# Performance work log

Hardware: AMD Instinct MI355X
Metric: run time of the kernel (lower is better)

## Reference

```python
import jax, jax.numpy as jnp
import numpy as np

NUM_NODES = 100000
OUT_CHANNELS = 32
NUM_EDGES = 3200000


def setup_inputs() -> dict:
    key = jax.random.key(0)
    k1, k2, k3 = jax.random.split(key, 3)
    edge_index = jax.random.randint(k1, (2, NUM_EDGES), 0, NUM_NODES, dtype=jnp.int64)
    # nn.Linear init: weight [out, in], uniform(-1/sqrt(in), 1/sqrt(in))
    bound = 1.0 / np.sqrt(NUM_NODES)
    W = jax.random.uniform(k2, (OUT_CHANNELS, NUM_NODES), jnp.float32, -bound, bound)
    b = jax.random.uniform(k3, (OUT_CHANNELS,), jnp.float32, -bound, bound)
    return {"edge_index": edge_index, "W": W, "b": b}


def reference(edge_index, W, b):
    # LINK forward: A = sparse COO [N, num_nodes] with 1.0 per edge (duplicates sum),
    # logits = A @ W.T + b. Implemented as gather + segment_sum (no dense A).
    row = edge_index[0]
    col = edge_index[1]
    row = row - row.min()  # faithful to `row = row - row.min()`
    gathered = jnp.take(W.T, col, axis=0)  # [E, out_channels]
    logits = jax.ops.segment_sum(gathered, row, num_segments=NUM_NODES)  # [N, out]
    return logits + b
```

## Files before the change

### kernel.cpp

```cpp
#include <hip/hip_runtime.h>

#define NUM_NODES 100000
#define OUT_CH 32
#define NUM_EDGES 3200000

#define RPB 128
#define NB 782
#define CAP2 5120
#define TPB 512
#define TILE 12800
#define KPT 25
#define NTILE 250
#define TR_BLOCKS 3125
#define MIN_BLOCKS 256

static __device__ __forceinline__ unsigned short f32_to_bf16_rne(float f) {
    unsigned u = __float_as_uint(f);
    unsigned r = u + 0x7FFFu + ((u >> 16) & 1u);
    return (unsigned short)(r >> 16);
}
static __device__ __forceinline__ float bf16_to_f32(unsigned short h) {
    return __uint_as_float(((unsigned)h) << 16);
}

__global__ void __launch_bounds__(256)
fused_pre(const float* __restrict__ W, ushort4* __restrict__ Wt,
          const int4* __restrict__ row4, int* __restrict__ partmin,
          int* __restrict__ bcount) {
    int bk = blockIdx.x;
    int t  = threadIdx.x;
    if (bk < TR_BLOCKS) {
        __shared__ float tile[32][33];
        int tx = t & 31, ty = t >> 5;
        int colBase = bk * 32;
        #pragma unroll
        for (int k = 0; k < 4; k++) {
            int c = ty + 8 * k;
            tile[c][tx] = W[c * NUM_NODES + colBase + tx];
        }
        __syncthreads();
        int lc = t >> 3, q = t & 7;
        ushort4 o;
        o.x = f32_to_bf16_rne(tile[q * 4 + 0][lc]);
        o.y = f32_to_bf16_rne(tile[q * 4 + 1][lc]);
        o.z = f32_to_bf16_rne(tile[q * 4 + 2][lc]);
        o.w = f32_to_bf16_rne(tile[q * 4 + 3][lc]);
        Wt[(size_t)(colBase + lc) * 8 + q] = o;
    } else if (bk < TR_BLOCKS + MIN_BLOCKS) {
        int mb  = bk - TR_BLOCKS;
        int tid = mb * 256 + t;
        int m = 0x7fffffff;
        for (int i = tid; i < NUM_EDGES / 4; i += MIN_BLOCKS * 256) {
            int4 v = row4[i];
            m = min(m, min(min(v.x, v.y), min(v.z, v.w)));
        }
        #pragma unroll
        for (int off = 32; off > 0; off >>= 1) m = min(m, __shfl_down(m, off, 64));
        __shared__ int wm[4];
        if ((t & 63) == 0) wm[t >> 6] = m;
        __syncthreads();
        if (t == 0) partmin[mb] = min(min(wm[0], wm[1]), min(wm[2], wm[3]));
    } else {
        for (int i = t; i < NB; i += 256) bcount[i] = 0;
    }
}

__global__ void __launch_bounds__(TPB)
bin_stage(const int* __restrict__ edge, const int* __restrict__ partmin,
          int* __restrict__ bcount, unsigned int* __restrict__ bin) {
    __shared__ int cnt[NB];
    __shared__ int cur[NB];
    __shared__ int rminS;
    int t = threadIdx.x;
    if (t < 64) {
        int m = min(min(partmin[t], partmin[t + 64]),
                    min(partmin[t + 128], partmin[t + 192]));
        #pragma unroll
        for (int off = 32; off > 0; off >>= 1) m = min(m, __shfl_down(m, off, 64));
        if (t == 0) rminS = m;
    }
    for (int i = t; i < NB; i += TPB) cnt[i] = 0;
    __syncthreads();
    int rmin = rminS;
    int eb = blockIdx.x * TILE;

    unsigned int ent[KPT];
    int bb[KPT];
    #pragma unroll
    for (int k = 0; k < KPT; k++) {
        int e = eb + k * TPB + t;
        int r = edge[e] - rmin;
        int c = edge[NUM_EDGES + e];
        int b = r >> 7;
        bb[k]  = b;
        ent[k] = ((unsigned int)(r & 127) << 17) | (unsigned int)c;
        atomicAdd(&cnt[b], 1);
    }
    __syncthreads();

    for (int i = t; i < NB; i += TPB) cur[i] = cnt[i] ? atomicAdd(&bcount[i], cnt[i]) : 0;
    __syncthreads();

    #pragma unroll
    for (int k = 0; k < KPT; k++) {
        int pos = atomicAdd(&cur[bb[k]], 1);
        if (pos < CAP2) bin[(size_t)bb[k] * CAP2 + pos] = ent[k];
    }
}

__global__ void __launch_bounds__(TPB)
bucket_gather(const unsigned int* __restrict__ bin, const int* __restrict__ bcount,
              const ushort4* __restrict__ Wt, const float* __restrict__ b,
              float* __restrict__ out) {
    __shared__ int cnt2[RPB * 8];
    __shared__ int cur2[RPB * 8];
    __shared__ int rowstart[RPB];
    __shared__ int rowcnt[RPB];
    __shared__ int scn[RPB];
    __shared__ int lcol[CAP2];

    int t = threadIdx.x;
    int bk = blockIdx.x;
    int n = bcount[bk];
    if (n > CAP2) n = CAP2;
    const unsigned int* mybin = bin + (size_t)bk * CAP2;

    for (int i = t; i < RPB * 8; i += TPB) cnt2[i] = 0;
    __syncthreads();

    for (int i = t; i < n; i += TPB) {
        unsigned int p = mybin[i];
        int lr  = p >> 17;
        int seg = (p & 0x1FFFF) >> 14;
        atomicAdd(&cnt2[(lr << 3) | seg], 1);
    }
    __syncthreads();

    if (t < RPB) {
        int s = 0;
        #pragma unroll
        for (int k = 0; k < 8; k++) s += cnt2[(t << 3) | k];
        rowcnt[t] = s;
        scn[t] = s;
    }
    __syncthreads();
    for (int off = 1; off < RPB; off <<= 1) {
        int v = (t < RPB && t >= off) ? scn[t - off] : 0;
        __syncthreads();
        if (t < RPB) scn[t] += v;
        __syncthreads();
    }
    if (t < RPB) {
        int rs = scn[t] - rowcnt[t];
        rowstart[t] = rs;
        int run = rs;
        #pragma unroll
        for (int k = 0; k < 8; k++) { cur2[(t << 3) | k] = run; run += cnt2[(t << 3) | k]; }
    }
    __syncthreads();

    for (int i = t; i < n; i += TPB) {
        unsigned int p = mybin[i];
        int lr = p >> 17;
        int c  = p & 0x1FFFF;
        int pos = atomicAdd(&cur2[(lr << 3) | (c >> 14)], 1);
        lcol[pos] = c;
    }
    __syncthreads();

    int g   = t >> 3;
    int sub = t & 7;
    float4 bias = ((const float4*)b)[sub];
    for (int lr = g; lr < RPB; lr += 64) {
        int row = bk * RPB + lr;
        if (row >= NUM_NODES) break;
        int s = rowstart[lr];
        int e = s + rowcnt[lr];
        float4 acc = bias;
        for (int i = s; i < e; i++) {
            ushort4 w = Wt[(size_t)lcol[i] * 8 + sub];
            acc.x += bf16_to_f32(w.x);
            acc.y += bf16_to_f32(w.y);
            acc.z += bf16_to_f32(w.z);
            acc.w += bf16_to_f32(w.w);
        }
        ((float4*)out)[(size_t)row * 8 + sub] = acc;
    }
}

extern "C" void kernel_launch(void* const* d_in, const int* in_sizes, int n_in,
                              void* d_out, int out_size, void* d_ws, size_t ws_size,
                              hipStream_t stream) {
    const int*   edge = (const int*)d_in[0];
    const float* W    = (const float*)d_in[1];
    const float* b    = (const float*)d_in[2];
    float* out = (float*)d_out;

    char* ws = (char*)d_ws;
    int*          partmin = (int*)ws;
    int*          bcount  = (int*)(ws + 1024);
    ushort4*      Wt      = (ushort4*)(ws + 8192);
    unsigned int* bin     = (unsigned int*)(ws + 6422528);

    fused_pre<<<TR_BLOCKS + MIN_BLOCKS + 1, 256, 0, stream>>>(W, Wt, (const int4*)edge, partmin, bcount);
    bin_stage<<<NTILE, TPB, 0, stream>>>(edge, partmin, bcount, bin);
    bucket_gather<<<NB, TPB, 0, stream>>>(bin, bcount, Wt, b, out);
}
```

Before: 152.4 us.

## Use nontemporal loads/stores, widen bin stage to 1024 threads, cache bin entries in registers

Switches the edge reads, bin writes, bin reads and output stores to nontemporal builtins to reduce cache pollution. The bin stage now runs 1024 threads per block with 13 entries per thread and bounds checks. The bucket gather keeps its bin entries in registers (10 per thread) so the second pass does not re-read global memory. Nontemporal bin stores could hurt if the following kernel would have hit in L2, and the larger register arrays may lower occupancy.

```diff
diff --git a/kernel.cpp b/kernel.cpp
--- a/kernel.cpp
+++ b/kernel.cpp
@@ -7,12 +7,17 @@
 #define RPB 128
 #define NB 782
 #define CAP2 5120
+#define TPB_BIN 1024
+#define TILE 12800
+#define KPT 13
+#define NTILE 250
 #define TPB 512
-#define TILE 12800
-#define KPT 25
-#define NTILE 250
+#define EPT 10
 #define TR_BLOCKS 3125
 #define MIN_BLOCKS 256
+
+typedef int   nint4  __attribute__((ext_vector_type(4)));
+typedef float nfloat4 __attribute__((ext_vector_type(4)));
 
 static __device__ __forceinline__ unsigned short f32_to_bf16_rne(float f) {
     unsigned u = __float_as_uint(f);
@@ -25,7 +30,7 @@
 
 __global__ void __launch_bounds__(256)
 fused_pre(const float* __restrict__ W, ushort4* __restrict__ Wt,
-          const int4* __restrict__ row4, int* __restrict__ partmin,
+          const nint4* __restrict__ row4, int* __restrict__ partmin,
           int* __restrict__ bcount) {
     int bk = blockIdx.x;
     int t  = threadIdx.x;
@@ -51,7 +56,7 @@
         int tid = mb * 256 + t;
         int m = 0x7fffffff;
         for (int i = tid; i < NUM_EDGES / 4; i += MIN_BLOCKS * 256) {
-            int4 v = row4[i];
+            nint4 v = __builtin_nontemporal_load(&row4[i]);
             m = min(m, min(min(v.x, v.y), min(v.z, v.w)));
         }
         #pragma unroll
@@ -65,7 +70,7 @@
     }
 }
 
-__global__ void __launch_bounds__(TPB)
+__global__ void __launch_bounds__(TPB_BIN)
 bin_stage(const int* __restrict__ edge, const int* __restrict__ partmin,
           int* __restrict__ bcount, unsigned int* __restrict__ bin) {
     __shared__ int cnt[NB];
@@ -79,7 +84,7 @@
         for (int off = 32; off > 0; off >>= 1) m = min(m, __shfl_down(m, off, 64));
         if (t == 0) rminS = m;
     }
-    for (int i = t; i < NB; i += TPB) cnt[i] = 0;
+    for (int i = t; i < NB; i += TPB_BIN) cnt[i] = 0;
     __syncthreads();
     int rmin = rminS;
     int eb = blockIdx.x * TILE;
@@ -88,23 +93,29 @@
     int bb[KPT];
     #pragma unroll
     for (int k = 0; k < KPT; k++) {
-        int e = eb + k * TPB + t;
-        int r = edge[e] - rmin;
-        int c = edge[NUM_EDGES + e];
-        int b = r >> 7;
-        bb[k]  = b;
-        ent[k] = ((unsigned int)(r & 127) << 17) | (unsigned int)c;
-        atomicAdd(&cnt[b], 1);
-    }
-    __syncthreads();
-
-    for (int i = t; i < NB; i += TPB) cur[i] = cnt[i] ? atomicAdd(&bcount[i], cnt[i]) : 0;
+        int o = k * TPB_BIN + t;
+        bb[k] = -1;
+        if (o < TILE) {
+            int e = eb + o;
+            int r = __builtin_nontemporal_load(&edge[e]) - rmin;
+            int c = __builtin_nontemporal_load(&edge[NUM_EDGES + e]);
+            int b = r >> 7;
+            bb[k]  = b;
+            ent[k] = ((unsigned int)(r & 127) << 17) | (unsigned int)c;
+            atomicAdd(&cnt[b], 1);
+        }
+    }
+    __syncthreads();
+
+    for (int i = t; i < NB; i += TPB_BIN) cur[i] = cnt[i] ? atomicAdd(&bcount[i], cnt[i]) : 0;
     __syncthreads();
 
     #pragma unroll
     for (int k = 0; k < KPT; k++) {
-        int pos = atomicAdd(&cur[bb[k]], 1);
-        if (pos < CAP2) bin[(size_t)bb[k] * CAP2 + pos] = ent[k];
+        if (bb[k] >= 0) {
+            int pos = atomicAdd(&cur[bb[k]], 1);
+            if (pos < CAP2) __builtin_nontemporal_store(ent[k], &bin[(size_t)bb[k] * CAP2 + pos]);
+        }
     }
 }
 
@@ -128,11 +139,18 @@
     for (int i = t; i < RPB * 8; i += TPB) cnt2[i] = 0;
     __syncthreads();
 
-    for (int i = t; i < n; i += TPB) {
-        unsigned int p = mybin[i];
-        int lr  = p >> 17;
-        int seg = (p & 0x1FFFF) >> 14;
-        atomicAdd(&cnt2[(lr << 3) | seg], 1);
+    unsigned int ent[EPT];
+    #pragma unroll
+    for (int k = 0; k < EPT; k++) {
+        int i = t + k * TPB;
+        ent[k] = 0xFFFFFFFFu;
+        if (i < n) {
+            unsigned int p = __builtin_nontemporal_load(&mybin[i]);
+            ent[k] = p;
+            int lr  = p >> 17;
+            int seg = (p & 0x1FFFF) >> 14;
+            atomicAdd(&cnt2[(lr << 3) | seg], 1);
+        }
     }
     __syncthreads();
 
@@ -159,12 +177,15 @@
     }
     __syncthreads();
 
-    for (int i = t; i < n; i += TPB) {
-        unsigned int p = mybin[i];
-        int lr = p >> 17;
-        int c  = p & 0x1FFFF;
-        int pos = atomicAdd(&cur2[(lr << 3) | (c >> 14)], 1);
-        lcol[pos] = c;
+    #pragma unroll
+    for (int k = 0; k < EPT; k++) {
+        unsigned int p = ent[k];
+        if (p != 0xFFFFFFFFu) {
+            int lr = p >> 17;
+            int c  = p & 0x1FFFF;
+            int pos = atomicAdd(&cur2[(lr << 3) | (c >> 14)], 1);
+            lcol[pos] = c;
+        }
     }
     __syncthreads();
 
@@ -184,7 +205,8 @@
             acc.z += bf16_to_f32(w.z);
             acc.w += bf16_to_f32(w.w);
         }
-        ((float4*)out)[(size_t)row * 8 + sub] = acc;
+        nfloat4 o = { acc.x, acc.y, acc.z, acc.w };
+        __builtin_nontemporal_store(o, &((nfloat4*)out)[(size_t)row * 8 + sub]);
     }
 }
 
@@ -202,7 +224,7 @@
     ushort4*      Wt      = (ushort4*)(ws + 8192);
     unsigned int* bin     = (unsigned int*)(ws + 6422528);
 
-    fused_pre<<<TR_BLOCKS + MIN_BLOCKS + 1, 256, 0, stream>>>(W, Wt, (const int4*)edge, partmin, bcount);
-    bin_stage<<<NTILE, TPB, 0, stream>>>(edge, partmin, bcount, bin);
+    fused_pre<<<TR_BLOCKS + MIN_BLOCKS + 1, 256, 0, stream>>>(W, Wt, (const nint4*)edge, partmin, bcount);
+    bin_stage<<<NTILE, TPB_BIN, 0, stream>>>(edge, partmin, bcount, bin);
     bucket_gather<<<NB, TPB, 0, stream>>>(bin, bcount, Wt, b, out);
 }
```

Result: slower. 231.2 us (+51.7%).
